# Optimization experiments

Measured on AMD Instinct MI355X. Metric: run time of the kernel, lower is better.

## Reference

```python
import jax, jax.numpy as jnp
import numpy as np

SC, ST, B, D, H, E, F, TOPK = 2048, 2048, 4, 256, 4, 8, 1024, 2
AUXW = 0.01
EPS = 1e-5


def setup_inputs() -> dict:
    key = jax.random.key(0)
    ks = jax.random.split(key, 16)
    s = 0.02
    n = lambda k, shp: (jax.random.normal(k, shp, jnp.float32) * s)
    z = lambda shp: jnp.zeros(shp, jnp.float32)
    o = lambda shp: jnp.ones(shp, jnp.float32)
    return {
        "x_context": jax.random.normal(ks[0], (SC, B, D), jnp.float32),
        "x_target": jax.random.normal(ks[1], (ST, B, D), jnp.float32),
        # shared self/cross attention (separate_att=False)
        "Wq": n(ks[2], (D, D)), "Wk": n(ks[3], (D, D)), "Wv": n(ks[4], (D, D)),
        "bq": z(D), "bk": z(D), "bv": z(D),
        "Wo": n(ks[5], (D, D)), "bo": z(D),
        # MoE gating + stacked 2-layer expert MLPs (D -> F -> D)
        "Wg": n(ks[6], (D, E)), "bg": z(E),
        "W1": n(ks[7], (E, D, F)), "b1": z((E, F)),
        "W2": n(ks[8], (E, F, D)), "b2": z((E, D)),
        # four post-LayerNorms
        "g_c1": o(D), "b_c1": z(D), "g_c2": o(D), "b_c2": z(D),
        "g_t1": o(D), "b_t1": z(D), "g_t2": o(D), "b_t2": z(D),
    }


def _ln(x, g, b):
    mu = x.mean(-1, keepdims=True)
    var = ((x - mu) ** 2).mean(-1, keepdims=True)
    return (x - mu) * jax.lax.rsqrt(var + EPS) * g + b


def _mha(q_in, kv, Wq, Wk, Wv, bq, bk, bv, Wo, bo):
    Sq, Bt, Dm = q_in.shape
    Sk = kv.shape[0]
    dh = Dm // H
    q = (q_in @ Wq + bq).reshape(Sq, Bt, H, dh)
    k = (kv @ Wk + bk).reshape(Sk, Bt, H, dh)
    v = (kv @ Wv + bv).reshape(Sk, Bt, H, dh)
    scores = jnp.einsum('qbhd,kbhd->bhqk', q, k) / jnp.asarray(np.sqrt(dh), q.dtype)
    attn = jax.nn.softmax(scores, axis=-1)
    out = jnp.einsum('bhqk,kbhd->qbhd', attn, v).reshape(Sq, Bt, Dm)
    return out @ Wo + bo


def _moe(x, Wg, bg, W1, b1, W2, b2):
    shp = x.shape
    xf = x.reshape(-1, shp[-1])          # [T, D]
    T = xf.shape[0]
    probs = jax.nn.softmax(xf @ Wg + bg, axis=-1)   # [T, E]
    gv, gi = jax.lax.top_k(probs, TOPK)
    gv = gv / gv.sum(-1, keepdims=True)
    # dense combine weights: gate value if expert selected else 0
    comb = jnp.zeros((T, E), xf.dtype).at[jnp.arange(T)[:, None], gi].add(gv)
    out = jnp.zeros_like(xf)
    for e in range(E):                    # fixed small expert loop
        h = jax.nn.relu(xf @ W1[e] + b1[e])
        out = out + (h @ W2[e] + b2[e]) * comb[:, e:e + 1]
    counts = probs.sum(0)
    frac = counts / counts.sum()
    aux = E * jnp.sum(frac * probs.mean(0))
    return out.reshape(shp), aux


def reference(x_context, x_target, Wq, Wk, Wv, bq, bk, bv, Wo, bo,
              Wg, bg, W1, b1, W2, b2,
              g_c1, b_c1, g_c2, b_c2, g_t1, b_t1, g_t2, b_t2):
    # context self-attention (post-norm)
    a = _mha(x_context, x_context, Wq, Wk, Wv, bq, bk, bv, Wo, bo)
    xc = _ln(a + x_context, g_c1, b_c1)
    f, aux1 = _moe(xc, Wg, bg, W1, b1, W2, b2)
    xc = _ln(f + xc, g_c2, b_c2)
    # target cross-attention over context (shared attention weights)
    a = _mha(x_target, xc, Wq, Wk, Wv, bq, bk, bv, Wo, bo)
    xt = _ln(a + x_target, g_t1, b_t1)
    f, aux2 = _moe(xt, Wg, bg, W1, b1, W2, b2)
    xt = _ln(f + xt, g_t2, b_t2)
    aux = AUXW * (aux1 + aux2)
    return xc, xt, aux
```

## Files before the change

kernel.cpp:

```cpp
#include <hip/hip_runtime.h>
#include <hip/hip_bf16.h>

typedef _Float16 f16_t;
typedef _Float16 f16x8 __attribute__((ext_vector_type(8)));
typedef float f32x4 __attribute__((ext_vector_type(4)));

template<bool BIAS, bool OUTF16>
__global__ __launch_bounds__(256) void gemm16_kernel(
    const f16_t* __restrict__ A, const f16_t* __restrict__ B, void* __restrict__ Cv,
    const float* __restrict__ bias, int M, int N, int K, int lda, int ldb, int ldc)
{
    __shared__ f16_t As[64][72];
    __shared__ f16_t Bs[64][72];
    const int m0 = blockIdx.y * 64, n0 = blockIdx.x * 64;
    const int t = threadIdx.x, wave = t >> 6, lane = t & 63;
    const int wr = (wave >> 1) * 32, wc = (wave & 1) * 32;
    const int lr = lane & 15, kg = lane >> 4;
    const int sr = t >> 2, sc = (t & 3) * 16;
    const f16_t* arp = A + (long long)(m0 + sr) * lda;
    const f16_t* brp = B + (long long)(n0 + sr) * ldb;

    f32x4 acc[2][2] = {};
    for (int k0 = 0; k0 < K; k0 += 64) {
        *reinterpret_cast<f16x8*>(&As[sr][sc])     = *reinterpret_cast<const f16x8*>(&arp[k0 + sc]);
        *reinterpret_cast<f16x8*>(&As[sr][sc + 8]) = *reinterpret_cast<const f16x8*>(&arp[k0 + sc + 8]);
        *reinterpret_cast<f16x8*>(&Bs[sr][sc])     = *reinterpret_cast<const f16x8*>(&brp[k0 + sc]);
        *reinterpret_cast<f16x8*>(&Bs[sr][sc + 8]) = *reinterpret_cast<const f16x8*>(&brp[k0 + sc + 8]);
        __syncthreads();
        #pragma unroll
        for (int c = 0; c < 2; c++) {
            f16x8 a0 = *reinterpret_cast<const f16x8*>(&As[wr + lr][c * 32 + kg * 8]);
            f16x8 a1 = *reinterpret_cast<const f16x8*>(&As[wr + 16 + lr][c * 32 + kg * 8]);
            f16x8 b0 = *reinterpret_cast<const f16x8*>(&Bs[wc + lr][c * 32 + kg * 8]);
            f16x8 b1 = *reinterpret_cast<const f16x8*>(&Bs[wc + 16 + lr][c * 32 + kg * 8]);
            acc[0][0] = __builtin_amdgcn_mfma_f32_16x16x32_f16(a0, b0, acc[0][0], 0, 0, 0);
            acc[0][1] = __builtin_amdgcn_mfma_f32_16x16x32_f16(a0, b1, acc[0][1], 0, 0, 0);
            acc[1][0] = __builtin_amdgcn_mfma_f32_16x16x32_f16(a1, b0, acc[1][0], 0, 0, 0);
            acc[1][1] = __builtin_amdgcn_mfma_f32_16x16x32_f16(a1, b1, acc[1][1], 0, 0, 0);
        }
        __syncthreads();
    }
    #pragma unroll
    for (int mi = 0; mi < 2; mi++)
        #pragma unroll
        for (int ni = 0; ni < 2; ni++)
            #pragma unroll
            for (int r = 0; r < 4; r++) {
                const int row = m0 + wr + mi * 16 + kg * 4 + r;
                const int col = n0 + wc + ni * 16 + lr;
                float v = acc[mi][ni][r];
                if constexpr (BIAS) v += bias[col];
                if constexpr (OUTF16) ((f16_t*)Cv)[(long long)row * ldc + col] = (f16_t)v;
                else                  ((float*)Cv)[(long long)row * ldc + col] = v;
            }
}

template<bool GATHER, bool RELU, bool OUTF16>
__global__ __launch_bounds__(256) void moe_gemm16_kernel(
    const f16_t* __restrict__ A, const int* __restrict__ tok_of_slot,
    const f16_t* __restrict__ W, const float* __restrict__ bias,
    void* __restrict__ Cv, const int* __restrict__ ebase,
    int N, int K, int lda, int ldb, int ldc, int wstride, int bstride)
{
    const int m0 = blockIdx.y * 64;
    if (m0 >= ebase[8]) return;
    int e = 0;
    #pragma unroll
    for (int i = 1; i < 8; i++) if (m0 >= ebase[i]) e = i;
    const f16_t* __restrict__ B = W + (long long)e * wstride;
    const float* __restrict__ bs = bias + e * bstride;

    __shared__ f16_t As[64][72];
    __shared__ f16_t Bs[64][72];
    const int n0 = blockIdx.x * 64;
    const int t = threadIdx.x, wave = t >> 6, lane = t & 63;
    const int wr = (wave >> 1) * 32, wc = (wave & 1) * 32;
    const int lr = lane & 15, kg = lane >> 4;
    const int sr = t >> 2, sc = (t & 3) * 16;
    const f16_t* arp;
    if constexpr (GATHER) arp = A + (long long)tok_of_slot[m0 + sr] * lda;
    else                  arp = A + (long long)(m0 + sr) * lda;
    const f16_t* brp = B + (long long)(n0 + sr) * ldb;

    f32x4 acc[2][2] = {};
    for (int k0 = 0; k0 < K; k0 += 64) {
        *reinterpret_cast<f16x8*>(&As[sr][sc])     = *reinterpret_cast<const f16x8*>(&arp[k0 + sc]);
        *reinterpret_cast<f16x8*>(&As[sr][sc + 8]) = *reinterpret_cast<const f16x8*>(&arp[k0 + sc + 8]);
        *reinterpret_cast<f16x8*>(&Bs[sr][sc])     = *reinterpret_cast<const f16x8*>(&brp[k0 + sc]);
        *reinterpret_cast<f16x8*>(&Bs[sr][sc + 8]) = *reinterpret_cast<const f16x8*>(&brp[k0 + sc + 8]);
        __syncthreads();
        #pragma unroll
        for (int c = 0; c < 2; c++) {
            f16x8 a0 = *reinterpret_cast<const f16x8*>(&As[wr + lr][c * 32 + kg * 8]);
            f16x8 a1 = *reinterpret_cast<const f16x8*>(&As[wr + 16 + lr][c * 32 + kg * 8]);
            f16x8 b0 = *reinterpret_cast<const f16x8*>(&Bs[wc + lr][c * 32 + kg * 8]);
            f16x8 b1 = *reinterpret_cast<const f16x8*>(&Bs[wc + 16 + lr][c * 32 + kg * 8]);
            acc[0][0] = __builtin_amdgcn_mfma_f32_16x16x32_f16(a0, b0, acc[0][0], 0, 0, 0);
            acc[0][1] = __builtin_amdgcn_mfma_f32_16x16x32_f16(a0, b1, acc[0][1], 0, 0, 0);
            acc[1][0] = __builtin_amdgcn_mfma_f32_16x16x32_f16(a1, b0, acc[1][0], 0, 0, 0);
            acc[1][1] = __builtin_amdgcn_mfma_f32_16x16x32_f16(a1, b1, acc[1][1], 0, 0, 0);
        }
        __syncthreads();
    }
    #pragma unroll
    for (int mi = 0; mi < 2; mi++)
        #pragma unroll
        for (int ni = 0; ni < 2; ni++)
            #pragma unroll
            for (int r = 0; r < 4; r++) {
                const int row = m0 + wr + mi * 16 + kg * 4 + r;
                const int col = n0 + wc + ni * 16 + lr;
                float v = acc[mi][ni][r] + bs[col];
                if constexpr (RELU) v = fmaxf(v, 0.f);
                if constexpr (OUTF16) ((f16_t*)Cv)[(long long)row * ldc + col] = (f16_t)v;
                else                  ((float*)Cv)[(long long)row * ldc + col] = v;
            }
}

__global__ __launch_bounds__(256) void flash_kernel(
    const f16_t* __restrict__ Q16, const f16_t* __restrict__ K16,
    const f16_t* __restrict__ V16, f16_t* __restrict__ O16)
{
    __shared__ f16_t Ks[64][72];
    __shared__ f16_t VsT[64][72];
    __shared__ f16_t Ps[4][16][72];

    const int z = blockIdx.y;
    const int m0 = blockIdx.x * 64;
    const int t = threadIdx.x, w = t >> 6, lane = t & 63;
    const int lr = lane & 15, kg = lane >> 4;
    const long long cbase = 64LL * z;

    f16x8 qf0, qf1;
    {
        const long long qrow = (long long)(m0 + w * 16 + lr) * 1024 + cbase;
        qf0 = *reinterpret_cast<const f16x8*>(&Q16[qrow + kg * 8]);
        qf1 = *reinterpret_cast<const f16x8*>(&Q16[qrow + 32 + kg * 8]);
    }

    f32x4 oacc[4] = {};
    float mrun[4] = { -1e30f, -1e30f, -1e30f, -1e30f };
    float lrun[4] = {};

    const int sr = t >> 2, sc = (t & 3) * 16;
    for (int n0 = 0; n0 < 2048; n0 += 64) {
        const long long krow = (long long)(n0 + sr) * 1024 + cbase;
        f16x8 kv0 = *reinterpret_cast<const f16x8*>(&K16[krow + sc]);
        f16x8 kv1 = *reinterpret_cast<const f16x8*>(&K16[krow + sc + 8]);
        f16x8 vv0 = *reinterpret_cast<const f16x8*>(&V16[krow + sc]);
        f16x8 vv1 = *reinterpret_cast<const f16x8*>(&V16[krow + sc + 8]);
        *reinterpret_cast<f16x8*>(&Ks[sr][sc])     = kv0;
        *reinterpret_cast<f16x8*>(&Ks[sr][sc + 8]) = kv1;
        #pragma unroll
        for (int i = 0; i < 8; i++) {
            VsT[sc + i][sr]     = vv0[i];
            VsT[sc + 8 + i][sr] = vv1[i];
        }
        __syncthreads();

        float sv[4][4];
        #pragma unroll
        for (int nt = 0; nt < 4; nt++) {
            f32x4 acc = {};
            f16x8 b0 = *reinterpret_cast<const f16x8*>(&Ks[nt * 16 + lr][kg * 8]);
            f16x8 b1 = *reinterpret_cast<const f16x8*>(&Ks[nt * 16 + lr][32 + kg * 8]);
            acc = __builtin_amdgcn_mfma_f32_16x16x32_f16(qf0, b0, acc, 0, 0, 0);
            acc = __builtin_amdgcn_mfma_f32_16x16x32_f16(qf1, b1, acc, 0, 0, 0);
            #pragma unroll
            for (int r = 0; r < 4; r++) sv[nt][r] = acc[r] * 0.125f;
        }

        float mnew[4], alpha[4];
        #pragma unroll
        for (int r = 0; r < 4; r++) {
            float rm = fmaxf(fmaxf(sv[0][r], sv[1][r]), fmaxf(sv[2][r], sv[3][r]));
            rm = fmaxf(rm, __shfl_xor(rm, 1));
            rm = fmaxf(rm, __shfl_xor(rm, 2));
            rm = fmaxf(rm, __shfl_xor(rm, 4));
            rm = fmaxf(rm, __shfl_xor(rm, 8));
            mnew[r] = fmaxf(mrun[r], rm);
            alpha[r] = __expf(mrun[r] - mnew[r]);
            mrun[r] = mnew[r];
        }
        #pragma unroll
        for (int nt = 0; nt < 4; nt++)
            #pragma unroll
            for (int r = 0; r < 4; r++) sv[nt][r] = __expf(sv[nt][r] - mnew[r]);
        #pragma unroll
        for (int r = 0; r < 4; r++) {
            float rs = sv[0][r] + sv[1][r] + sv[2][r] + sv[3][r];
            rs += __shfl_xor(rs, 1);
            rs += __shfl_xor(rs, 2);
            rs += __shfl_xor(rs, 4);
            rs += __shfl_xor(rs, 8);
            lrun[r] = lrun[r] * alpha[r] + rs;
        }
        #pragma unroll
        for (int dt = 0; dt < 4; dt++)
            #pragma unroll
            for (int r = 0; r < 4; r++) oacc[dt][r] *= alpha[r];

        #pragma unroll
        for (int nt = 0; nt < 4; nt++)
            #pragma unroll
            for (int r = 0; r < 4; r++)
                Ps[w][kg * 4 + r][nt * 16 + lr] = (f16_t)sv[nt][r];

        f16x8 pa0 = *reinterpret_cast<const f16x8*>(&Ps[w][lr][kg * 8]);
        f16x8 pa1 = *reinterpret_cast<const f16x8*>(&Ps[w][lr][32 + kg * 8]);
        #pragma unroll
        for (int dt = 0; dt < 4; dt++) {
            f16x8 vb0 = *reinterpret_cast<const f16x8*>(&VsT[dt * 16 + lr][kg * 8]);
            f16x8 vb1 = *reinterpret_cast<const f16x8*>(&VsT[dt * 16 + lr][32 + kg * 8]);
            oacc[dt] = __builtin_amdgcn_mfma_f32_16x16x32_f16(pa0, vb0, oacc[dt], 0, 0, 0);
            oacc[dt] = __builtin_amdgcn_mfma_f32_16x16x32_f16(pa1, vb1, oacc[dt], 0, 0, 0);
        }
        __syncthreads();
    }

    const long long orow0 = (long long)(m0 + w * 16) * 1024 + cbase;
    #pragma unroll
    for (int r = 0; r < 4; r++) {
        const float inv = 1.f / lrun[r];
        #pragma unroll
        for (int dt = 0; dt < 4; dt++)
            O16[orow0 + (long long)(kg * 4 + r) * 1024 + dt * 16 + lr] =
                (f16_t)(oacc[dt][r] * inv);
    }
}

__global__ __launch_bounds__(256) void wtrans_kernel(
    const float* __restrict__ in, f16_t* __restrict__ out, int R, int C)
{
    __shared__ float tile[32][33];
    const long long zoff = (long long)blockIdx.z * R * C;
    const int r0 = blockIdx.y * 32, c0 = blockIdx.x * 32;
    const int tx = threadIdx.x & 31, ty = threadIdx.x >> 5;
    #pragma unroll
    for (int i = 0; i < 32; i += 8)
        tile[ty + i][tx] = in[zoff + (long long)(r0 + ty + i) * C + c0 + tx];
    __syncthreads();
    #pragma unroll
    for (int i = 0; i < 32; i += 8)
        out[zoff + (long long)(c0 + ty + i) * R + r0 + tx] = (f16_t)tile[tx][ty + i];
}

__global__ __launch_bounds__(256) void cvt16_kernel(
    const float* __restrict__ in, f16_t* __restrict__ out)
{
    const long long i = ((long long)blockIdx.x * 256 + threadIdx.x) * 4;
    float4 v = *reinterpret_cast<const float4*>(&in[i]);
    f16_t o[4] = { (f16_t)v.x, (f16_t)v.y, (f16_t)v.z, (f16_t)v.w };
    *reinterpret_cast<ulong1*>(&out[i]) = *reinterpret_cast<ulong1*>(o);
}

__global__ __launch_bounds__(256) void ln_kernel(
    const float* __restrict__ in1, const float* __restrict__ in2,
    const float* __restrict__ gamma, const float* __restrict__ beta,
    float* __restrict__ out, f16_t* __restrict__ out16)
{
    const int wave = threadIdx.x >> 6, lane = threadIdx.x & 63;
    const long long row = (long long)blockIdx.x * 4 + wave;
    const long long base = row * 256 + lane * 4;
    float4 a = *reinterpret_cast<const float4*>(&in1[base]);
    float4 b = *reinterpret_cast<const float4*>(&in2[base]);
    float x[4] = { a.x + b.x, a.y + b.y, a.z + b.z, a.w + b.w };
    float s = x[0] + x[1] + x[2] + x[3];
    float s2 = x[0]*x[0] + x[1]*x[1] + x[2]*x[2] + x[3]*x[3];
    #pragma unroll
    for (int o = 32; o; o >>= 1) { s += __shfl_xor(s, o); s2 += __shfl_xor(s2, o); }
    const float mean = s * (1.f / 256.f);
    const float var = s2 * (1.f / 256.f) - mean * mean;
    const float rstd = rsqrtf(var + 1e-5f);
    float4 g = *reinterpret_cast<const float4*>(&gamma[lane * 4]);
    float4 bb = *reinterpret_cast<const float4*>(&beta[lane * 4]);
    const float* gf = reinterpret_cast<const float*>(&g);
    const float* bf = reinterpret_cast<const float*>(&bb);
    float y[4];
    #pragma unroll
    for (int i = 0; i < 4; i++) y[i] = (x[i] - mean) * rstd * gf[i] + bf[i];
    *reinterpret_cast<float4*>(&out[base]) = make_float4(y[0], y[1], y[2], y[3]);
    if (out16) {
        f16_t o[4] = { (f16_t)y[0], (f16_t)y[1], (f16_t)y[2], (f16_t)y[3] };
        *reinterpret_cast<ulong1*>(&out16[base]) = *reinterpret_cast<ulong1*>(o);
    }
}

__global__ __launch_bounds__(256) void gating_kernel(
    const float* __restrict__ X, const float* __restrict__ Wg, const float* __restrict__ bg,
    int* __restrict__ gcount, float* __restrict__ counts,
    int* __restrict__ pos_of_tok, int* __restrict__ exp_of_tok,
    float* __restrict__ gate_of_tok)
{
    __shared__ float WgL[2048];
    __shared__ float cpart[8];
    __shared__ int lcnt[8];
    __shared__ int lbase[8];
    const int t = threadIdx.x;
    for (int i = t; i < 2048; i += 256) WgL[i] = Wg[i];
    if (t < 8) { cpart[t] = 0.f; lcnt[t] = 0; }
    __syncthreads();

    const int tok = blockIdx.x * 256 + t;
    const float* xr = X + (long long)tok * 256;
    float acc[8] = {};
    for (int k = 0; k < 256; k += 4) {
        float4 xv = *reinterpret_cast<const float4*>(xr + k);
        const float* xf = reinterpret_cast<const float*>(&xv);
        #pragma unroll
        for (int i = 0; i < 4; i++) {
            const float xi = xf[i];
            const float* wrow = &WgL[(k + i) * 8];
            #pragma unroll
            for (int e = 0; e < 8; e++) acc[e] += xi * wrow[e];
        }
    }
    float p[8]; float mx = -1e30f;
    #pragma unroll
    for (int e = 0; e < 8; e++) { p[e] = acc[e] + bg[e]; mx = fmaxf(mx, p[e]); }
    float se = 0.f;
    #pragma unroll
    for (int e = 0; e < 8; e++) { p[e] = __expf(p[e] - mx); se += p[e]; }
    const float inv = 1.f / se;
    #pragma unroll
    for (int e = 0; e < 8; e++) { p[e] *= inv; atomicAdd(&cpart[e], p[e]); }

    int i1 = 0;
    #pragma unroll
    for (int e = 1; e < 8; e++) if (p[e] > p[i1]) i1 = e;
    int i2 = (i1 == 0) ? 1 : 0;
    #pragma unroll
    for (int e = 0; e < 8; e++) if (e != i1 && p[e] > p[i2]) i2 = e;
    const float gs = 1.f / (p[i1] + p[i2]);

    const int p1 = atomicAdd(&lcnt[i1], 1);
    const int p2 = atomicAdd(&lcnt[i2], 1);
    __syncthreads();
    if (t < 8) {
        lbase[t] = atomicAdd(&gcount[t], lcnt[t]);
        atomicAdd(&counts[t], cpart[t]);
    }
    __syncthreads();
    pos_of_tok[2 * tok]     = lbase[i1] + p1;
    pos_of_tok[2 * tok + 1] = lbase[i2] + p2;
    exp_of_tok[2 * tok]     = i1;
    exp_of_tok[2 * tok + 1] = i2;
    gate_of_tok[2 * tok]     = p[i1] * gs;
    gate_of_tok[2 * tok + 1] = p[i2] * gs;
}

__global__ void finalize_kernel(const int* __restrict__ gcount, int* __restrict__ ebase)
{
    if (threadIdx.x == 0) {
        int b = 0;
        for (int e = 0; e < 8; e++) { ebase[e] = b; b += (gcount[e] + 63) & ~63; }
        ebase[8] = b;
    }
}

__global__ __launch_bounds__(256) void scatter_kernel(
    const int* __restrict__ pos_of_tok, const int* __restrict__ exp_of_tok,
    const int* __restrict__ ebase, int* __restrict__ tok_of_slot)
{
    const int i = blockIdx.x * 256 + threadIdx.x;
    const int e = exp_of_tok[i];
    tok_of_slot[ebase[e] + pos_of_tok[i]] = i >> 1;
}

__global__ __launch_bounds__(256) void moe_combine_ln_kernel(
    const float* __restrict__ Ys, const float* __restrict__ X1,
    const int* __restrict__ pos_of_tok, const int* __restrict__ exp_of_tok,
    const float* __restrict__ gate_of_tok, const int* __restrict__ ebase,
    const float* __restrict__ gamma, const float* __restrict__ beta,
    float* __restrict__ out, f16_t* __restrict__ out16)
{
    const int wave = threadIdx.x >> 6, lane = threadIdx.x & 63;
    const long long tok = (long long)blockIdx.x * 4 + wave;
    const int e1 = exp_of_tok[2 * tok], e2 = exp_of_tok[2 * tok + 1];
    const long long s1 = ebase[e1] + pos_of_tok[2 * tok];
    const long long s2 = ebase[e2] + pos_of_tok[2 * tok + 1];
    const float gv1 = gate_of_tok[2 * tok], gv2 = gate_of_tok[2 * tok + 1];
    const long long base = tok * 256 + lane * 4;
    float4 y1 = *reinterpret_cast<const float4*>(&Ys[s1 * 256 + lane * 4]);
    float4 y2 = *reinterpret_cast<const float4*>(&Ys[s2 * 256 + lane * 4]);
    float4 xv = *reinterpret_cast<const float4*>(&X1[base]);
    float x[4] = { gv1 * y1.x + gv2 * y2.x + xv.x,
                   gv1 * y1.y + gv2 * y2.y + xv.y,
                   gv1 * y1.z + gv2 * y2.z + xv.z,
                   gv1 * y1.w + gv2 * y2.w + xv.w };
    float s = x[0] + x[1] + x[2] + x[3];
    float s2v = x[0]*x[0] + x[1]*x[1] + x[2]*x[2] + x[3]*x[3];
    #pragma unroll
    for (int o = 32; o; o >>= 1) { s += __shfl_xor(s, o); s2v += __shfl_xor(s2v, o); }
    const float mean = s * (1.f / 256.f);
    const float var = s2v * (1.f / 256.f) - mean * mean;
    const float rstd = rsqrtf(var + 1e-5f);
    float4 g = *reinterpret_cast<const float4*>(&gamma[lane * 4]);
    float4 bb = *reinterpret_cast<const float4*>(&beta[lane * 4]);
    const float* gf = reinterpret_cast<const float*>(&g);
    const float* bf = reinterpret_cast<const float*>(&bb);
    float y[4];
    #pragma unroll
    for (int i = 0; i < 4; i++) y[i] = (x[i] - mean) * rstd * gf[i] + bf[i];
    *reinterpret_cast<float4*>(&out[base]) = make_float4(y[0], y[1], y[2], y[3]);
    if (out16) {
        f16_t o[4] = { (f16_t)y[0], (f16_t)y[1], (f16_t)y[2], (f16_t)y[3] };
        *reinterpret_cast<ulong1*>(&out16[base]) = *reinterpret_cast<ulong1*>(o);
    }
}

__global__ void aux_kernel(const float* __restrict__ counts, float* __restrict__ out)
{
    if (threadIdx.x == 0) {
        float aux = 0.f;
        for (int pzz = 0; pzz < 2; pzz++) {
            const float* c = counts + pzz * 8;
            float tot = 0.f;
            for (int e = 0; e < 8; e++) tot += c[e];
            float s = 0.f;
            for (int e = 0; e < 8; e++) s += (c[e] / tot) * (c[e] * (1.f / 8192.f));
            aux += 8.f * s;
        }
        out[0] = 0.01f * aux;
    }
}

extern "C" void kernel_launch(void* const* d_in, const int* in_sizes, int n_in,
                              void* d_out, int out_size, void* d_ws, size_t ws_size,
                              hipStream_t stream)
{
    const float* Xc  = (const float*)d_in[0];
    const float* Xt  = (const float*)d_in[1];
    const float* Wq  = (const float*)d_in[2];
    const float* Wk  = (const float*)d_in[3];
    const float* Wv  = (const float*)d_in[4];
    const float* bq  = (const float*)d_in[5];
    const float* bk  = (const float*)d_in[6];
    const float* bv  = (const float*)d_in[7];
    const float* Wo  = (const float*)d_in[8];
    const float* bo  = (const float*)d_in[9];
    const float* Wg  = (const float*)d_in[10];
    const float* bg  = (const float*)d_in[11];
    const float* W1  = (const float*)d_in[12];
    const float* b1  = (const float*)d_in[13];
    const float* W2  = (const float*)d_in[14];
    const float* b2  = (const float*)d_in[15];
    const float* g_c1 = (const float*)d_in[16];
    const float* b_c1 = (const float*)d_in[17];
    const float* g_c2 = (const float*)d_in[18];
    const float* b_c2 = (const float*)d_in[19];
    const float* g_t1 = (const float*)d_in[20];
    const float* b_t1 = (const float*)d_in[21];
    const float* g_t2 = (const float*)d_in[22];
    const float* b_t2 = (const float*)d_in[23];

    const long long NTOK = 2097152;
    const int SLOT_MAX = 16896;
    float* dout = (float*)d_out;
    float* xcout = dout;
    float* xtout = dout + NTOK;

    float* ws = (float*)d_ws;
    float* P1 = ws;
    float* X1 = P1 + NTOK;
    float* Ys = X1 + NTOK;
    float* counts      = Ys + (long long)SLOT_MAX * 256;
    float* gate_of_tok = counts + 16;
    int* gcount      = (int*)(gate_of_tok + 16384);
    int* ebase       = gcount + 16;
    int* pos_of_tok  = ebase + 16;
    int* exp_of_tok  = pos_of_tok + 16384;
    int* tok_of_slot = exp_of_tok + 16384;
    f16_t* h16 = (f16_t*)(tok_of_slot + SLOT_MAX);
    f16_t* Xc16 = h16;
    f16_t* Xt16 = Xc16 + NTOK;
    f16_t* xc16 = Xt16 + NTOK;
    f16_t* Q16  = xc16 + NTOK;
    f16_t* K16  = Q16 + NTOK;
    f16_t* V16  = K16 + NTOK;
    f16_t* O16  = V16 + NTOK;
    f16_t* X116 = O16 + NTOK;
    f16_t* Hs16 = X116 + NTOK;
    f16_t* WqT  = Hs16 + (long long)SLOT_MAX * 1024;
    f16_t* WkT  = WqT + 65536;
    f16_t* WvT  = WkT + 65536;
    f16_t* WoT  = WvT + 65536;
    f16_t* W1T  = WoT + 65536;
    f16_t* W2T  = W1T + 2097152;

    hipMemsetAsync(counts, 0, 16 * sizeof(float), stream);
    hipMemsetAsync(gcount, 0, 16 * sizeof(int), stream);

    cvt16_kernel<<<2048, 256, 0, stream>>>(Xc, Xc16);
    cvt16_kernel<<<2048, 256, 0, stream>>>(Xt, Xt16);
    wtrans_kernel<<<dim3(8, 8, 1), 256, 0, stream>>>(Wq, WqT, 256, 256);
    wtrans_kernel<<<dim3(8, 8, 1), 256, 0, stream>>>(Wk, WkT, 256, 256);
    wtrans_kernel<<<dim3(8, 8, 1), 256, 0, stream>>>(Wv, WvT, 256, 256);
    wtrans_kernel<<<dim3(8, 8, 1), 256, 0, stream>>>(Wo, WoT, 256, 256);
    wtrans_kernel<<<dim3(32, 8, 8), 256, 0, stream>>>(W1, W1T, 256, 1024);
    wtrans_kernel<<<dim3(8, 32, 8), 256, 0, stream>>>(W2, W2T, 1024, 256);

    for (int pass = 0; pass < 2; pass++) {
        const float*  xq    = pass ? Xt   : Xc;
        const f16_t*  xq16  = pass ? Xt16 : Xc16;
        const f16_t*  xkv16 = pass ? xc16 : Xc16;
        const float* g1  = pass ? g_t1 : g_c1;
        const float* be1 = pass ? b_t1 : b_c1;
        const float* g2  = pass ? g_t2 : g_c2;
        const float* be2 = pass ? b_t2 : b_c2;
        float* cnt = counts + pass * 8;
        int* gcnt  = gcount + pass * 8;
        float* oln = pass ? xtout : xcout;
        f16_t* oln16 = pass ? nullptr : xc16;

        gemm16_kernel<true,true><<<dim3(4,128), 256, 0, stream>>>(
            xq16,  WqT, Q16, bq, 8192, 256, 256, 256, 256, 256);
        gemm16_kernel<true,true><<<dim3(4,128), 256, 0, stream>>>(
            xkv16, WkT, K16, bk, 8192, 256, 256, 256, 256, 256);
        gemm16_kernel<true,true><<<dim3(4,128), 256, 0, stream>>>(
            xkv16, WvT, V16, bv, 8192, 256, 256, 256, 256, 256);

        flash_kernel<<<dim3(32, 16), 256, 0, stream>>>(Q16, K16, V16, O16);

        gemm16_kernel<true,false><<<dim3(4,128), 256, 0, stream>>>(
            O16, WoT, P1, bo, 8192, 256, 256, 256, 256, 256);
        ln_kernel<<<2048, 256, 0, stream>>>(P1, xq, g1, be1, X1, X116);

        hipMemsetAsync(tok_of_slot, 0, SLOT_MAX * sizeof(int), stream);
        gating_kernel<<<32, 256, 0, stream>>>(X1, Wg, bg, gcnt, cnt,
                                              pos_of_tok, exp_of_tok, gate_of_tok);
        finalize_kernel<<<1, 64, 0, stream>>>(gcnt, ebase);
        scatter_kernel<<<64, 256, 0, stream>>>(pos_of_tok, exp_of_tok, ebase, tok_of_slot);
        moe_gemm16_kernel<true,true,true><<<dim3(16, 264), 256, 0, stream>>>(
            X116, tok_of_slot, W1T, b1, Hs16, ebase,
            1024, 256, 256, 256, 1024, 262144, 1024);
        moe_gemm16_kernel<false,false,false><<<dim3(4, 264), 256, 0, stream>>>(
            Hs16, nullptr, W2T, b2, Ys, ebase,
            256, 1024, 1024, 1024, 256, 262144, 256);
        moe_combine_ln_kernel<<<2048, 256, 0, stream>>>(
            Ys, X1, pos_of_tok, exp_of_tok, gate_of_tok, ebase, g2, be2, oln, oln16);
    }

    aux_kernel<<<1, 64, 0, stream>>>(counts, dout + 2 * NTOK);
}
```

Baseline: 637.7 us.

## Split attention over key chunks, pre-transpose V, and fuse QKV projections

Fuses the three Q/K/V projection GEMMs into one launch using a z-dimension selector. V is pre-transposed by a separate kernel so flash attention loads it with vector reads instead of scalar transposed LDS stores. The flash kernel is split into four key-range chunks (split-K) to raise occupancy from 512 to 2048 blocks, writing fp32 partial outputs plus running max and sum, which a merge kernel then combines. The softmax scale is also folded into Q. This adds extra fp32 partial-output traffic and two extra launches, and it reuses the Hs16 buffer for the partials.

```diff
diff --git a/kernel.cpp b/kernel.cpp
--- a/kernel.cpp
+++ b/kernel.cpp
@@ -52,6 +52,60 @@
                 if constexpr (BIAS) v += bias[col];
                 if constexpr (OUTF16) ((f16_t*)Cv)[(long long)row * ldc + col] = (f16_t)v;
                 else                  ((float*)Cv)[(long long)row * ldc + col] = v;
+            }
+}
+
+__global__ __launch_bounds__(256) void qkv_kernel(
+    const f16_t* __restrict__ Aq, const f16_t* __restrict__ Akv,
+    const f16_t* __restrict__ B0, const f16_t* __restrict__ B1, const f16_t* __restrict__ B2,
+    const float* __restrict__ bi0, const float* __restrict__ bi1, const float* __restrict__ bi2,
+    f16_t* __restrict__ C0, f16_t* __restrict__ C1, f16_t* __restrict__ C2)
+{
+    const int zz = blockIdx.z;
+    const f16_t* A = (zz == 0) ? Aq : Akv;
+    const f16_t* B = (zz == 0) ? B0 : (zz == 1 ? B1 : B2);
+    const float* bias = (zz == 0) ? bi0 : (zz == 1 ? bi1 : bi2);
+    f16_t* C = (zz == 0) ? C0 : (zz == 1 ? C1 : C2);
+
+    __shared__ f16_t As[64][72];
+    __shared__ f16_t Bs[64][72];
+    const int m0 = blockIdx.y * 64, n0 = blockIdx.x * 64;
+    const int t = threadIdx.x, wave = t >> 6, lane = t & 63;
+    const int wr = (wave >> 1) * 32, wc = (wave & 1) * 32;
+    const int lr = lane & 15, kg = lane >> 4;
+    const int sr = t >> 2, sc = (t & 3) * 16;
+    const f16_t* arp = A + (long long)(m0 + sr) * 256;
+    const f16_t* brp = B + (long long)(n0 + sr) * 256;
+
+    f32x4 acc[2][2] = {};
+    for (int k0 = 0; k0 < 256; k0 += 64) {
+        *reinterpret_cast<f16x8*>(&As[sr][sc])     = *reinterpret_cast<const f16x8*>(&arp[k0 + sc]);
+        *reinterpret_cast<f16x8*>(&As[sr][sc + 8]) = *reinterpret_cast<const f16x8*>(&arp[k0 + sc + 8]);
+        *reinterpret_cast<f16x8*>(&Bs[sr][sc])     = *reinterpret_cast<const f16x8*>(&brp[k0 + sc]);
+        *reinterpret_cast<f16x8*>(&Bs[sr][sc + 8]) = *reinterpret_cast<const f16x8*>(&brp[k0 + sc + 8]);
+        __syncthreads();
+        #pragma unroll
+        for (int c = 0; c < 2; c++) {
+            f16x8 a0 = *reinterpret_cast<const f16x8*>(&As[wr + lr][c * 32 + kg * 8]);
+            f16x8 a1 = *reinterpret_cast<const f16x8*>(&As[wr + 16 + lr][c * 32 + kg * 8]);
+            f16x8 b0 = *reinterpret_cast<const f16x8*>(&Bs[wc + lr][c * 32 + kg * 8]);
+            f16x8 b1 = *reinterpret_cast<const f16x8*>(&Bs[wc + 16 + lr][c * 32 + kg * 8]);
+            acc[0][0] = __builtin_amdgcn_mfma_f32_16x16x32_f16(a0, b0, acc[0][0], 0, 0, 0);
+            acc[0][1] = __builtin_amdgcn_mfma_f32_16x16x32_f16(a0, b1, acc[0][1], 0, 0, 0);
+            acc[1][0] = __builtin_amdgcn_mfma_f32_16x16x32_f16(a1, b0, acc[1][0], 0, 0, 0);
+            acc[1][1] = __builtin_amdgcn_mfma_f32_16x16x32_f16(a1, b1, acc[1][1], 0, 0, 0);
+        }
+        __syncthreads();
+    }
+    #pragma unroll
+    for (int mi = 0; mi < 2; mi++)
+        #pragma unroll
+        for (int ni = 0; ni < 2; ni++)
+            #pragma unroll
+            for (int r = 0; r < 4; r++) {
+                const int row = m0 + wr + mi * 16 + kg * 4 + r;
+                const int col = n0 + wc + ni * 16 + lr;
+                C[(long long)row * 256 + col] = (f16_t)(acc[mi][ni][r] + bias[col]);
             }
 }
 
@@ -117,15 +171,33 @@
             }
 }
 
+__global__ __launch_bounds__(256) void vtrans_kernel(
+    const f16_t* __restrict__ V16, f16_t* __restrict__ VT)
+{
+    __shared__ f16_t tile[32][33];
+    const int z = blockIdx.z;
+    const int s0 = blockIdx.x * 32, d0 = blockIdx.y * 32;
+    const int tx = threadIdx.x & 31, ty = threadIdx.x >> 5;
+    #pragma unroll
+    for (int i = 0; i < 32; i += 8)
+        tile[ty + i][tx] = V16[(long long)(s0 + ty + i) * 1024 + 64 * z + d0 + tx];
+    __syncthreads();
+    #pragma unroll
+    for (int i = 0; i < 32; i += 8)
+        VT[(long long)z * 131072 + (long long)(d0 + ty + i) * 2048 + s0 + tx] = tile[tx][ty + i];
+}
+
 __global__ __launch_bounds__(256) void flash_kernel(
     const f16_t* __restrict__ Q16, const f16_t* __restrict__ K16,
-    const f16_t* __restrict__ V16, f16_t* __restrict__ O16)
+    const f16_t* __restrict__ VT, float* __restrict__ Opart,
+    float* __restrict__ mlm, float* __restrict__ mll)
 {
     __shared__ f16_t Ks[64][72];
-    __shared__ f16_t VsT[64][72];
+    __shared__ f16_t VTs[64][72];
     __shared__ f16_t Ps[4][16][72];
 
     const int z = blockIdx.y;
+    const int c = blockIdx.z;
     const int m0 = blockIdx.x * 64;
     const int t = threadIdx.x, w = t >> 6, lane = t & 63;
     const int lr = lane & 15, kg = lane >> 4;
@@ -136,6 +208,8 @@
         const long long qrow = (long long)(m0 + w * 16 + lr) * 1024 + cbase;
         qf0 = *reinterpret_cast<const f16x8*>(&Q16[qrow + kg * 8]);
         qf1 = *reinterpret_cast<const f16x8*>(&Q16[qrow + 32 + kg * 8]);
+        #pragma unroll
+        for (int i = 0; i < 8; i++) { qf0[i] *= (f16_t)0.125f; qf1[i] *= (f16_t)0.125f; }
     }
 
     f32x4 oacc[4] = {};
@@ -143,19 +217,14 @@
     float lrun[4] = {};
 
     const int sr = t >> 2, sc = (t & 3) * 16;
-    for (int n0 = 0; n0 < 2048; n0 += 64) {
+    const int nbeg = c * 512;
+    for (int n0 = nbeg; n0 < nbeg + 512; n0 += 64) {
         const long long krow = (long long)(n0 + sr) * 1024 + cbase;
-        f16x8 kv0 = *reinterpret_cast<const f16x8*>(&K16[krow + sc]);
-        f16x8 kv1 = *reinterpret_cast<const f16x8*>(&K16[krow + sc + 8]);
-        f16x8 vv0 = *reinterpret_cast<const f16x8*>(&V16[krow + sc]);
-        f16x8 vv1 = *reinterpret_cast<const f16x8*>(&V16[krow + sc + 8]);
-        *reinterpret_cast<f16x8*>(&Ks[sr][sc])     = kv0;
-        *reinterpret_cast<f16x8*>(&Ks[sr][sc + 8]) = kv1;
-        #pragma unroll
-        for (int i = 0; i < 8; i++) {
-            VsT[sc + i][sr]     = vv0[i];
-            VsT[sc + 8 + i][sr] = vv1[i];
-        }
+        const long long vrow = (long long)z * 131072 + (long long)sr * 2048 + n0;
+        *reinterpret_cast<f16x8*>(&Ks[sr][sc])      = *reinterpret_cast<const f16x8*>(&K16[krow + sc]);
+        *reinterpret_cast<f16x8*>(&Ks[sr][sc + 8])  = *reinterpret_cast<const f16x8*>(&K16[krow + sc + 8]);
+        *reinterpret_cast<f16x8*>(&VTs[sr][sc])     = *reinterpret_cast<const f16x8*>(&VT[vrow + sc]);
+        *reinterpret_cast<f16x8*>(&VTs[sr][sc + 8]) = *reinterpret_cast<const f16x8*>(&VT[vrow + sc + 8]);
         __syncthreads();
 
         float sv[4][4];
@@ -167,7 +236,7 @@
             acc = __builtin_amdgcn_mfma_f32_16x16x32_f16(qf0, b0, acc, 0, 0, 0);
             acc = __builtin_amdgcn_mfma_f32_16x16x32_f16(qf1, b1, acc, 0, 0, 0);
             #pragma unroll
-            for (int r = 0; r < 4; r++) sv[nt][r] = acc[r] * 0.125f;
+            for (int r = 0; r < 4; r++) sv[nt][r] = acc[r];
         }
 
         float mnew[4], alpha[4];
@@ -210,23 +279,62 @@
         f16x8 pa1 = *reinterpret_cast<const f16x8*>(&Ps[w][lr][32 + kg * 8]);
         #pragma unroll
         for (int dt = 0; dt < 4; dt++) {
-            f16x8 vb0 = *reinterpret_cast<const f16x8*>(&VsT[dt * 16 + lr][kg * 8]);
-            f16x8 vb1 = *reinterpret_cast<const f16x8*>(&VsT[dt * 16 + lr][32 + kg * 8]);
+            f16x8 vb0 = *reinterpret_cast<const f16x8*>(&VTs[dt * 16 + lr][kg * 8]);
+            f16x8 vb1 = *reinterpret_cast<const f16x8*>(&VTs[dt * 16 + lr][32 + kg * 8]);
             oacc[dt] = __builtin_amdgcn_mfma_f32_16x16x32_f16(pa0, vb0, oacc[dt], 0, 0, 0);
             oacc[dt] = __builtin_amdgcn_mfma_f32_16x16x32_f16(pa1, vb1, oacc[dt], 0, 0, 0);
         }
         __syncthreads();
     }
 
+    float* op = Opart + (long long)c * 2097152;
     const long long orow0 = (long long)(m0 + w * 16) * 1024 + cbase;
     #pragma unroll
-    for (int r = 0; r < 4; r++) {
-        const float inv = 1.f / lrun[r];
+    for (int r = 0; r < 4; r++)
         #pragma unroll
         for (int dt = 0; dt < 4; dt++)
-            O16[orow0 + (long long)(kg * 4 + r) * 1024 + dt * 16 + lr] =
-                (f16_t)(oacc[dt][r] * inv);
-    }
+            op[orow0 + (long long)(kg * 4 + r) * 1024 + dt * 16 + lr] = oacc[dt][r];
+    if (lr == 0) {
+        const int b = z >> 2, h = z & 3;
+        #pragma unroll
+        for (int r = 0; r < 4; r++) {
+            const int tok = (m0 + w * 16 + kg * 4 + r) * 4 + b;
+            const long long idx = (long long)(c * 4 + h) * 8192 + tok;
+            mlm[idx] = mrun[r];
+            mll[idx] = lrun[r];
+        }
+    }
+}
+
+__global__ __launch_bounds__(256) void merge_kernel(
+    const float* __restrict__ Opart, const float* __restrict__ mlm,
+    const float* __restrict__ mll, f16_t* __restrict__ O16)
+{
+    const int w = threadIdx.x >> 6, lane = threadIdx.x & 63;
+    const int trow = blockIdx.x * 4 + w;
+    const int h = lane >> 4;
+    float m[4], l[4];
+    #pragma unroll
+    for (int c = 0; c < 4; c++) {
+        m[c] = mlm[(long long)(c * 4 + h) * 8192 + trow];
+        l[c] = mll[(long long)(c * 4 + h) * 8192 + trow];
+    }
+    float M = fmaxf(fmaxf(m[0], m[1]), fmaxf(m[2], m[3]));
+    float wv[4], L = 0.f;
+    #pragma unroll
+    for (int c = 0; c < 4; c++) { wv[c] = __expf(m[c] - M); L += wv[c] * l[c]; }
+    const float inv = 1.f / L;
+    const long long base = (long long)trow * 256 + lane * 4;
+    float4 acc = make_float4(0.f, 0.f, 0.f, 0.f);
+    #pragma unroll
+    for (int c = 0; c < 4; c++) {
+        float4 v = *reinterpret_cast<const float4*>(&Opart[(long long)c * 2097152 + base]);
+        acc.x += wv[c] * v.x; acc.y += wv[c] * v.y;
+        acc.z += wv[c] * v.z; acc.w += wv[c] * v.w;
+    }
+    f16_t o[4] = { (f16_t)(acc.x * inv), (f16_t)(acc.y * inv),
+                   (f16_t)(acc.z * inv), (f16_t)(acc.w * inv) };
+    *reinterpret_cast<ulong1*>(&O16[base]) = *reinterpret_cast<ulong1*>(o);
 }
 
 __global__ __launch_bounds__(256) void wtrans_kernel(
@@ -466,7 +574,9 @@
     float* Ys = X1 + NTOK;
     float* counts      = Ys + (long long)SLOT_MAX * 256;
     float* gate_of_tok = counts + 16;
-    int* gcount      = (int*)(gate_of_tok + 16384);
+    float* mlm = gate_of_tok + 16384;
+    float* mll = mlm + 131072;
+    int* gcount      = (int*)(mll + 131072);
     int* ebase       = gcount + 16;
     int* pos_of_tok  = ebase + 16;
     int* exp_of_tok  = pos_of_tok + 16384;
@@ -480,13 +590,15 @@
     f16_t* V16  = K16 + NTOK;
     f16_t* O16  = V16 + NTOK;
     f16_t* X116 = O16 + NTOK;
-    f16_t* Hs16 = X116 + NTOK;
+    f16_t* VT   = X116 + NTOK;
+    f16_t* Hs16 = VT + NTOK;
     f16_t* WqT  = Hs16 + (long long)SLOT_MAX * 1024;
     f16_t* WkT  = WqT + 65536;
     f16_t* WvT  = WkT + 65536;
     f16_t* WoT  = WvT + 65536;
     f16_t* W1T  = WoT + 65536;
     f16_t* W2T  = W1T + 2097152;
+    float* Opart = (float*)Hs16;
 
     hipMemsetAsync(counts, 0, 16 * sizeof(float), stream);
     hipMemsetAsync(gcount, 0, 16 * sizeof(int), stream);
@@ -513,16 +625,14 @@
         float* oln = pass ? xtout : xcout;
         f16_t* oln16 = pass ? nullptr : xc16;
 
-        gemm16_kernel<true,true><<<dim3(4,128), 256, 0, stream>>>(
-            xq16,  WqT, Q16, bq, 8192, 256, 256, 256, 256, 256);
-        gemm16_kernel<true,true><<<dim3(4,128), 256, 0, stream>>>(
-            xkv16, WkT, K16, bk, 8192, 256, 256, 256, 256, 256);
-        gemm16_kernel<true,true><<<dim3(4,128), 256, 0, stream>>>(
-            xkv16, WvT, V16, bv, 8192, 256, 256, 256, 256, 256);
-
-        flash_kernel<<<dim3(32, 16), 256, 0, stream>>>(Q16, K16, V16, O16);
-
-        gemm16_kernel<true,false><<<dim3(4,128), 256, 0, stream>>>(
+        qkv_kernel<<<dim3(4, 128, 3), 256, 0, stream>>>(
+            xq16, xkv16, WqT, WkT, WvT, bq, bk, bv, Q16, K16, V16);
+
+        vtrans_kernel<<<dim3(64, 2, 16), 256, 0, stream>>>(V16, VT);
+        flash_kernel<<<dim3(32, 16, 4), 256, 0, stream>>>(Q16, K16, VT, Opart, mlm, mll);
+        merge_kernel<<<2048, 256, 0, stream>>>(Opart, mlm, mll, O16);
+
+        gemm16_kernel<true,false><<<dim3(4, 128), 256, 0, stream>>>(
             O16, WoT, P1, bo, 8192, 256, 256, 256, 256, 256);
         ln_kernel<<<2048, 256, 0, stream>>>(P1, xq, g1, be1, X1, X116);
 
```

Measured after the change: 591.8 us. 7.2% less time.
